# Kernel optimization log

Measured on AMD Instinct MI355X. Metric: run time of the kernel, lower is better.

The kernel has to match this reference:

```python
import jax, jax.numpy as jnp
import numpy as np

B, DZ, H, DY = 4096, 512, 2048, 10
N_STEPS = 64
SCALE = 0.02  # matches param_ulow/uhigh magnitude


def setup_inputs() -> dict:
    key = jax.random.key(0)
    ks = jax.random.split(key, 6)
    x = jax.random.normal(ks[0], (B, DZ), dtype=jnp.float32)
    A = jax.random.normal(ks[1], (DZ, DZ), dtype=jnp.float32) * SCALE
    W1 = jax.random.normal(ks[2], (H, DZ), dtype=jnp.float32) * SCALE
    b1 = jax.random.normal(ks[3], (H,), dtype=jnp.float32) * SCALE
    W2 = jax.random.normal(ks[4], (DY, H), dtype=jnp.float32) * SCALE
    b2 = jax.random.normal(ks[5], (DY,), dtype=jnp.float32) * SCALE
    return {"x": x, "A": A, "W1": W1, "b1": b1, "W2": W2, "b2": b2,
            "n_steps": N_STEPS}


def reference(x, A, W1, b1, W2, b2, n_steps):
    # Z0 = P @ x with P = I  => Z0 = x
    # dz/dt = einsum('ji,bi->bj', A, z) = z @ A.T ; explicit Euler on [0, 1]
    dt = jnp.float32(1.0 / n_steps)

    def euler_step(z, _):
        return z + dt * (z @ A.T), None

    zT, _ = jax.lax.scan(euler_step, x, None, length=n_steps)  # [B, DZ]
    # Q MLP (n_layers=3): Linear -> ReLU -> Linear
    h = jax.nn.relu(zT @ W1.T + b1)  # [B, H]
    y = h @ W2.T + b2                # [B, DY]
    return y
```

## Files before the change

### kernel.cpp

```cpp
#include <hip/hip_runtime.h>
#include <hip/hip_bf16.h>

#define B_SZ 4096
#define DZ   512
#define H_SZ 2048
#define DY   10

#define C2 0.4921875f
#define C3 0.158935546875f
#define C4 0.037872314453125f
#define C5 ((float)(7624512.0/1073741824.0))
#define C6 ((float)(74974368.0/68719476736.0))

typedef __attribute__((ext_vector_type(8))) __bf16 bf16x8;
typedef __attribute__((ext_vector_type(4))) float  f32x4;
typedef __attribute__((ext_vector_type(8))) unsigned short us8;

__device__ inline unsigned short f2bf(float f) {
    unsigned u = __float_as_uint(f);
    u += 0x7fffu + ((u >> 16) & 1u);
    return (unsigned short)(u >> 16);
}
__device__ inline float bf2f(unsigned short s) {
    return __uint_as_float(((unsigned)s) << 16);
}

__device__ __forceinline__ void gl16(const void* g, void* l) {
    __builtin_amdgcn_global_load_lds(
        (const __attribute__((address_space(1))) unsigned int*)(size_t)g,
        (__attribute__((address_space(3))) unsigned int*)(unsigned)(size_t)l,
        16, 0, 0);
}

union SqSmem {
    struct { unsigned short A[64 * 64]; unsigned short B[64 * 64]; } s;
    float epi[64 * 68];
};

__device__ __forceinline__ void stage64(const unsigned short* __restrict__ src,
                                        unsigned short* lds, int row_base,
                                        int kt, int t) {
    const int w = t >> 6, lane = t & 63;
#pragma unroll
    for (int i = 0; i < 2; ++i) {
        int o = w * 128 + i * 64 + lane;
        int row = o >> 3, cc = (o & 7) ^ (row & 7);
        gl16(&src[(size_t)(row_base + row) * 512 + kt * 64 + cc * 8],
             &lds[(size_t)(w * 128 + i * 64) * 8]);
    }
}

#define MFMA_STEP(acc)                                                        \
    {                                                                         \
        _Pragma("unroll")                                                     \
        for (int ks = 0; ks < 2; ++ks) {                                      \
            bf16x8 af[2], bfr[2];                                             \
            _Pragma("unroll")                                                 \
            for (int i = 0; i < 2; ++i) {                                     \
                int ra = wm + i * 16 + l16, ca = (ks * 4 + quad) ^ (ra & 7);  \
                af[i] = *(const bf16x8*)&sm.s.A[ra * 64 + ca * 8];            \
                int rb = wn + i * 16 + l16, cb = (ks * 4 + quad) ^ (rb & 7);  \
                bfr[i] = *(const bf16x8*)&sm.s.B[rb * 64 + cb * 8];           \
            }                                                                 \
            _Pragma("unroll")                                                 \
            for (int i = 0; i < 2; ++i)                                       \
                _Pragma("unroll")                                             \
                for (int j = 0; j < 2; ++j)                                   \
                    acc[i][j] = __builtin_amdgcn_mfma_f32_16x16x32_bf16(      \
                        af[i], bfr[j], acc[i][j], 0, 0, 0);                   \
        }                                                                     \
    }

#define ACC_TO_EPI(acc)                                                       \
    {                                                                         \
        _Pragma("unroll")                                                     \
        for (int i = 0; i < 2; ++i)                                           \
            _Pragma("unroll")                                                 \
            for (int j = 0; j < 2; ++j)                                       \
                _Pragma("unroll")                                             \
                for (int rr = 0; rr < 4; ++rr)                                \
                    sm.epi[(wm + i * 16 + quad * 4 + rr) * 68 +               \
                           wn + j * 16 + l16] = acc[i][j][rr];                \
        __syncthreads();                                                      \
    }

__device__ inline void gemm64_mfma(const unsigned short* __restrict__ Arows,
                                   const unsigned short* __restrict__ Brows,
                                   int m0, int n0, int t, SqSmem& sm) {
    const int lane = t & 63, w = t >> 6, quad = lane >> 4, l16 = lane & 15;
    const int wm = (w & 1) * 32, wn = (w >> 1) * 32;
    f32x4 acc[2][2];
#pragma unroll
    for (int i = 0; i < 2; ++i)
#pragma unroll
        for (int j = 0; j < 2; ++j) acc[i][j] = (f32x4){0.f, 0.f, 0.f, 0.f};
    for (int kt = 0; kt < 8; ++kt) {
        stage64(Arows, sm.s.A, m0, kt, t);
        stage64(Brows, sm.s.B, n0, kt, t);
        __syncthreads();
        MFMA_STEP(acc)
        __syncthreads();
    }
    ACC_TO_EPI(acc)
}

__device__ inline void gemm64_f32src(const float* __restrict__ Arows,
                                     const float* __restrict__ Bsrc,
                                     int m0, int n0, int t, SqSmem& sm) {
    const int lane = t & 63, w = t >> 6, quad = lane >> 4, l16 = lane & 15;
    const int wm = (w & 1) * 32, wn = (w >> 1) * 32;
    const int r = t >> 2, cq = t & 3;
    f32x4 acc[2][2];
#pragma unroll
    for (int i = 0; i < 2; ++i)
#pragma unroll
        for (int j = 0; j < 2; ++j) acc[i][j] = (f32x4){0.f, 0.f, 0.f, 0.f};
    for (int kt = 0; kt < 8; ++kt) {
        float va[16];
#pragma unroll
        for (int u = 0; u < 4; ++u) {
            float4 f = *(const float4*)&Arows[(size_t)(m0 + r) * 512 + kt * 64 + cq * 16 + u * 4];
            va[u * 4 + 0] = f.x; va[u * 4 + 1] = f.y;
            va[u * 4 + 2] = f.z; va[u * 4 + 3] = f.w;
        }
#pragma unroll
        for (int j2 = 0; j2 < 2; ++j2) {
            us8 h;
#pragma unroll
            for (int j = 0; j < 8; ++j) h[j] = f2bf(va[j2 * 8 + j]);
            int cc = cq * 2 + j2;
            *(us8*)&sm.s.A[r * 64 + (cc ^ (r & 7)) * 8] = h;
        }
#pragma unroll
        for (int u = 0; u < 4; ++u) {
            float4 f = *(const float4*)&Bsrc[(size_t)(kt * 64 + r) * 512 + n0 + cq * 16 + u * 4];
            float vv[4] = {f.x, f.y, f.z, f.w};
#pragma unroll
            for (int j = 0; j < 4; ++j) {
                int n = cq * 16 + u * 4 + j;
                sm.s.B[n * 64 + ((r >> 3) ^ (n & 7)) * 8 + (r & 7)] = f2bf(vv[j]);
            }
        }
        __syncthreads();
        MFMA_STEP(acc)
        __syncthreads();
    }
    ACC_TO_EPI(acc)
}

__device__ inline void epi_out_bf(unsigned short* __restrict__ dst, int m0,
                                  int n0, int t, SqSmem& sm) {
    const int r = t >> 2, cq = t & 3;
    us8 h0, h1;
#pragma unroll
    for (int j = 0; j < 8; ++j) {
        h0[j] = f2bf(sm.epi[r * 68 + cq * 16 + j]);
        h1[j] = f2bf(sm.epi[r * 68 + cq * 16 + 8 + j]);
    }
    *(us8*)&dst[(size_t)(m0 + r) * 512 + n0 + cq * 16]     = h0;
    *(us8*)&dst[(size_t)(m0 + r) * 512 + n0 + cq * 16 + 8] = h1;
}
__device__ inline void epi_out_bfT(unsigned short* __restrict__ dst, int m0,
                                   int n0, int t, SqSmem& sm) {
    const int cf = t >> 2, rq = t & 3;
    us8 o0, o1;
#pragma unroll
    for (int i = 0; i < 8; ++i) {
        o0[i] = f2bf(sm.epi[(rq * 16 + i) * 68 + cf]);
        o1[i] = f2bf(sm.epi[(rq * 16 + 8 + i) * 68 + cf]);
    }
    *(us8*)&dst[(size_t)(n0 + cf) * 512 + m0 + rq * 16]     = o0;
    *(us8*)&dst[(size_t)(n0 + cf) * 512 + m0 + rq * 16 + 8] = o1;
}

__global__ __launch_bounds__(256) void k_s1(
    const float* __restrict__ A, const float* __restrict__ x,
    const float* __restrict__ W1, const float* __restrict__ b2,
    unsigned short* __restrict__ A2_bf, unsigned short* __restrict__ A2T_bf,
    unsigned short* __restrict__ AT_bf, unsigned short* __restrict__ x_bf,
    unsigned short* __restrict__ W1_bf, float* __restrict__ y) {
    __shared__ SqSmem sm;
    const int b = blockIdx.x, t = threadIdx.x;

    if (b < 64) {
        const int m0 = (b >> 3) * 64, n0 = (b & 7) * 64;
        gemm64_f32src(A, A, m0, n0, t, sm);
        epi_out_bf(A2_bf, m0, n0, t, sm);
        epi_out_bfT(A2T_bf, m0, n0, t, sm);
    } else if (b < 128) {
        const int bb = b - 64, m0 = (bb >> 3) * 64, n0 = (bb & 7) * 64;
        const int r = t >> 2, cq = t & 3;
#pragma unroll
        for (int u = 0; u < 4; ++u) {
            float4 f = *(const float4*)&A[(size_t)(m0 + r) * 512 + n0 + cq * 16 + u * 4];
            sm.epi[r * 68 + cq * 16 + u * 4 + 0] = f.x;
            sm.epi[r * 68 + cq * 16 + u * 4 + 1] = f.y;
            sm.epi[r * 68 + cq * 16 + u * 4 + 2] = f.z;
            sm.epi[r * 68 + cq * 16 + u * 4 + 3] = f.w;
        }
        __syncthreads();
        epi_out_bfT(AT_bf, m0, n0, t, sm);
    } else {
        const int gid = (b - 128) * 256 + t;
        const float4* x4 = (const float4*)x;
#pragma unroll
        for (int i = 0; i < 8; ++i) {
            int id = gid + i * 32768;
            float4 v0 = x4[(size_t)id * 2], v1 = x4[(size_t)id * 2 + 1];
            us8 o;
            o[0] = f2bf(v0.x); o[1] = f2bf(v0.y); o[2] = f2bf(v0.z); o[3] = f2bf(v0.w);
            o[4] = f2bf(v1.x); o[5] = f2bf(v1.y); o[6] = f2bf(v1.z); o[7] = f2bf(v1.w);
            *(us8*)&x_bf[(size_t)id * 8] = o;
        }
        const float4* w4 = (const float4*)W1;
#pragma unroll
        for (int i = 0; i < 4; ++i) {
            int id = gid + i * 32768;
            float4 v0 = w4[(size_t)id * 2], v1 = w4[(size_t)id * 2 + 1];
            us8 o;
            o[0] = f2bf(v0.x); o[1] = f2bf(v0.y); o[2] = f2bf(v0.z); o[3] = f2bf(v0.w);
            o[4] = f2bf(v1.x); o[5] = f2bf(v1.y); o[6] = f2bf(v1.z); o[7] = f2bf(v1.w);
            *(us8*)&W1_bf[(size_t)id * 8] = o;
        }
#pragma unroll
        for (int i = 0; i < 2; ++i) {
            int id = gid + i * 32768;
            if (id < B_SZ * DY) y[id] = b2[id % 10];
        }
    }
}

__global__ __launch_bounds__(256) void k_s2(
    const unsigned short* __restrict__ W1_bf,
    const unsigned short* __restrict__ A2_bf,
    const unsigned short* __restrict__ A2T_bf,
    const unsigned short* __restrict__ AT_bf,
    unsigned short* __restrict__ A4T_bf, unsigned short* __restrict__ U1_bf,
    unsigned short* __restrict__ U2_bf) {
    __shared__ SqSmem sm;
    const int b = blockIdx.x, t = threadIdx.x;
    if (b < 64) {
        const int m0 = (b >> 3) * 64, n0 = (b & 7) * 64;
        gemm64_mfma(A2T_bf, A2_bf, m0, n0, t, sm);
        epi_out_bf(A4T_bf, m0, n0, t, sm);
    } else if (b < 320) {
        const int bb = b - 64, m0 = (bb >> 3) * 64, n0 = (bb & 7) * 64;
        gemm64_mfma(W1_bf, AT_bf, m0, n0, t, sm);
        epi_out_bf(U1_bf, m0, n0, t, sm);
    } else {
        const int bb = b - 320, m0 = (bb >> 3) * 64, n0 = (bb & 7) * 64;
        gemm64_mfma(W1_bf, A2T_bf, m0, n0, t, sm);
        epi_out_bf(U2_bf, m0, n0, t, sm);
    }
}

__global__ __launch_bounds__(256) void k_s3(
    const float* __restrict__ W1, const unsigned short* __restrict__ U1_bf,
    const unsigned short* __restrict__ U2_bf,
    const unsigned short* __restrict__ A2T_bf,
    const unsigned short* __restrict__ A4T_bf,
    unsigned short* __restrict__ w1f) {
    __shared__ SqSmem sm;
    const int b = blockIdx.x, t = threadIdx.x;
    const int m0 = (b >> 3) * 64, n0 = (b & 7) * 64;
    const int lane = t & 63, w = t >> 6, quad = lane >> 4, l16 = lane & 15;
    const int wm = (w & 1) * 32, wn = (w >> 1) * 32;
    f32x4 acc[2][2];
#pragma unroll
    for (int i = 0; i < 2; ++i)
#pragma unroll
        for (int j = 0; j < 2; ++j) acc[i][j] = (f32x4){0.f, 0.f, 0.f, 0.f};

#pragma unroll
    for (int pass = 0; pass < 2; ++pass) {
        const unsigned short* __restrict__ Bt = pass ? A4T_bf : A2T_bf;
        const float c1c = pass ? C5 : C3;
        const float c2c = pass ? C6 : C4;
        for (int kt = 0; kt < 8; ++kt) {
            stage64(Bt, sm.s.B, n0, kt, t);
#pragma unroll
            for (int c = 0; c < 2; ++c) {
                int idx = c * 256 + t, row = idx >> 3, cc = idx & 7;
                int ccs = cc ^ (row & 7);
                size_t ga = (size_t)(m0 + row) * 512 + kt * 64 + cc * 8;
                us8 u1 = *(const us8*)&U1_bf[ga];
                us8 u2 = *(const us8*)&U2_bf[ga];
                us8 g;
#pragma unroll
                for (int j = 0; j < 8; ++j)
                    g[j] = f2bf(c1c * bf2f(u1[j]) + c2c * bf2f(u2[j]));
                *(us8*)&sm.s.A[row * 64 + ccs * 8] = g;
            }
            __syncthreads();
            MFMA_STEP(acc)
            __syncthreads();
        }
    }
    ACC_TO_EPI(acc)

    const int r = t >> 2, cq = t & 3;
    size_t gbase = (size_t)(m0 + r) * 512 + n0 + cq * 16;
    us8 u1a = *(const us8*)&U1_bf[gbase], u1b = *(const us8*)&U1_bf[gbase + 8];
    us8 u2a = *(const us8*)&U2_bf[gbase], u2b = *(const us8*)&U2_bf[gbase + 8];
    float4 wa = *(const float4*)&W1[gbase],      wbv = *(const float4*)&W1[gbase + 4];
    float4 wc = *(const float4*)&W1[gbase + 8],  wd  = *(const float4*)&W1[gbase + 12];
    float wf[16] = {wa.x, wa.y, wa.z, wa.w, wbv.x, wbv.y, wbv.z, wbv.w,
                    wc.x, wc.y, wc.z, wc.w, wd.x,  wd.y,  wd.z,  wd.w};
    us8 h0, h1;
#pragma unroll
    for (int j = 0; j < 8; ++j) {
        h0[j] = f2bf(wf[j] + bf2f(u1a[j]) + C2 * bf2f(u2a[j]) +
                     sm.epi[r * 68 + cq * 16 + j]);
        h1[j] = f2bf(wf[8 + j] + bf2f(u1b[j]) + C2 * bf2f(u2b[j]) +
                     sm.epi[r * 68 + cq * 16 + 8 + j]);
    }
    *(us8*)&w1f[gbase]     = h0;
    *(us8*)&w1f[gbase + 8] = h1;
}

union SmemU {
    struct { unsigned short A[128 * 64]; unsigned short B[128 * 64]; } s;
    struct { unsigned short h[128 * 136]; } e;
};

__global__ __launch_bounds__(256) void mlp_kernel(
    const unsigned short* __restrict__ x_bf,
    const unsigned short* __restrict__ w1f,
    const float* __restrict__ b1, const float* __restrict__ W2,
    float* __restrict__ y) {
    __shared__ SmemU sm;
    const int t    = threadIdx.x;
    const int lane = t & 63, w = t >> 6;
    const int quad = lane >> 4, l16 = lane & 15;
    const int wm = (w & 1) * 64, wn = (w >> 1) * 64;
    const int m0g = blockIdx.x * 128, n0g = blockIdx.y * 128;

    f32x4 acc[4][4];
#pragma unroll
    for (int i = 0; i < 4; ++i)
#pragma unroll
        for (int j = 0; j < 4; ++j) acc[i][j] = (f32x4){0.f, 0.f, 0.f, 0.f};

    for (int kt = 0; kt < 8; ++kt) {
#pragma unroll
        for (int i = 0; i < 4; ++i) {
            int o = w * 256 + i * 64 + lane;
            int row = o >> 3, cc = (o & 7) ^ (row & 7);
            gl16(&x_bf[(size_t)(m0g + row) * 512 + kt * 64 + cc * 8],
                 &sm.s.A[(size_t)(w * 256 + i * 64) * 8]);
        }
#pragma unroll
        for (int i = 0; i < 4; ++i) {
            int o = w * 256 + i * 64 + lane;
            int row = o >> 3, cc = (o & 7) ^ (row & 7);
            gl16(&w1f[(size_t)(n0g + row) * 512 + kt * 64 + cc * 8],
                 &sm.s.B[(size_t)(w * 256 + i * 64) * 8]);
        }
        __syncthreads();
#pragma unroll
        for (int ks = 0; ks < 2; ++ks) {
            bf16x8 af[4], bfr[4];
#pragma unroll
            for (int i = 0; i < 4; ++i) {
                int ra = wm + i * 16 + l16, ca = (ks * 4 + quad) ^ (ra & 7);
                af[i] = *(const bf16x8*)&sm.s.A[ra * 64 + ca * 8];
                int rb = wn + i * 16 + l16, cb = (ks * 4 + quad) ^ (rb & 7);
                bfr[i] = *(const bf16x8*)&sm.s.B[rb * 64 + cb * 8];
            }
#pragma unroll
            for (int i = 0; i < 4; ++i)
#pragma unroll
                for (int j = 0; j < 4; ++j)
                    acc[i][j] = __builtin_amdgcn_mfma_f32_16x16x32_bf16(
                        af[i], bfr[j], acc[i][j], 0, 0, 0);
        }
        __syncthreads();
    }

    float bias[4];
#pragma unroll
    for (int j = 0; j < 4; ++j) bias[j] = b1[n0g + wn + j * 16 + l16];
#pragma unroll
    for (int i = 0; i < 4; ++i)
#pragma unroll
        for (int j = 0; j < 4; ++j)
#pragma unroll
            for (int r = 0; r < 4; ++r) {
                float h = acc[i][j][r] + bias[j];
                h = h > 0.f ? h : 0.f;
                sm.e.h[(wm + i * 16 + quad * 4 + r) * 136 + wn + j * 16 + l16] =
                    f2bf(h);
            }
    __syncthreads();

    {
        bf16x8 wfrag[4];
#pragma unroll
        for (int kc = 0; kc < 4; ++kc) {
            us8 wb;
            if (l16 < DY) {
                const float* wp = &W2[(size_t)l16 * H_SZ + n0g + kc * 32 + quad * 8];
#pragma unroll
                for (int j = 0; j < 8; ++j) wb[j] = f2bf(wp[j]);
            } else {
#pragma unroll
                for (int j = 0; j < 8; ++j) wb[j] = 0;
            }
            wfrag[kc] = *(bf16x8*)&wb;
        }
#pragma unroll
        for (int hh = 0; hh < 2; ++hh) {
            const int mrow = w * 32 + hh * 16;
            f32x4 ay = (f32x4){0.f, 0.f, 0.f, 0.f};
#pragma unroll
            for (int kc = 0; kc < 4; ++kc) {
                bf16x8 af = *(const bf16x8*)&sm.e.h[(mrow + l16) * 136 +
                                                    kc * 32 + quad * 8];
                ay = __builtin_amdgcn_mfma_f32_16x16x32_bf16(af, wfrag[kc], ay,
                                                             0, 0, 0);
            }
            if (l16 < DY) {
#pragma unroll
                for (int r = 0; r < 4; ++r)
                    atomicAdd(&y[(size_t)(m0g + mrow + quad * 4 + r) * DY + l16],
                              ay[r]);
            }
        }
    }
}

extern "C" void kernel_launch(void* const* d_in, const int* in_sizes, int n_in,
                              void* d_out, int out_size, void* d_ws, size_t ws_size,
                              hipStream_t stream) {
    const float* x  = (const float*)d_in[0];
    const float* A  = (const float*)d_in[1];
    const float* W1 = (const float*)d_in[2];
    const float* b1 = (const float*)d_in[3];
    const float* W2 = (const float*)d_in[4];
    const float* b2 = (const float*)d_in[5];
    float* y = (float*)d_out;

    char* ws = (char*)d_ws;
    const size_t HMB = 512u * 1024, MB = 1u << 20;
    unsigned short* AT_bf  = (unsigned short*)(ws);
    unsigned short* A2_bf  = (unsigned short*)(ws + 1 * HMB);
    unsigned short* A2T_bf = (unsigned short*)(ws + 2 * HMB);
    unsigned short* A4T_bf = (unsigned short*)(ws + 3 * HMB);
    unsigned short* U1_bf  = (unsigned short*)(ws + 2 * MB);
    unsigned short* U2_bf  = (unsigned short*)(ws + 4 * MB);
    unsigned short* w1f    = (unsigned short*)(ws + 6 * MB);
    unsigned short* W1_bf  = (unsigned short*)(ws + 8 * MB);
    unsigned short* x_bf   = (unsigned short*)(ws + 10 * MB);

    k_s1<<<256, 256, 0, stream>>>(A, x, W1, b2, A2_bf, A2T_bf, AT_bf, x_bf,
                                  W1_bf, y);
    k_s2<<<576, 256, 0, stream>>>(W1_bf, A2_bf, A2T_bf, AT_bf, A4T_bf, U1_bf,
                                  U2_bf);
    k_s3<<<256, 256, 0, stream>>>(W1, U1_bf, U2_bf, A2T_bf, A4T_bf, w1f);
    mlp_kernel<<<dim3(32, 16), dim3(256), 0, stream>>>(x_bf, w1f, b1, W2, y);
}
```

Measured before the change: 140.7 us.

## Fold polynomial coefficients into a combined A-power matrix in k_s3

Adds an A^3 (transposed) product in k_s2 and changes k_s3 from two K-passes over U1/U2 to a single pass. The single pass multiplies U2 = W1·A^2 by a combined matrix C3·A + C4·A^2 + C5·A^3 + C6·A^4, built on the fly from the four bf16 A-power tiles. This halves the k_s3 MFMA loop and the per-tile U1/U2 loads. In exchange it adds 64 extra blocks to k_s2 and four small matrix reads per tile, and changes the bf16 rounding path.

After: 133.6 us. 5.1% less time.

```diff
diff --git a/kernel.cpp b/kernel.cpp
--- a/kernel.cpp
+++ b/kernel.cpp
@@ -232,23 +232,28 @@
 
 __global__ __launch_bounds__(256) void k_s2(
     const unsigned short* __restrict__ W1_bf,
+    const unsigned short* __restrict__ A_bfx,
     const unsigned short* __restrict__ A2_bf,
     const unsigned short* __restrict__ A2T_bf,
     const unsigned short* __restrict__ AT_bf,
-    unsigned short* __restrict__ A4T_bf, unsigned short* __restrict__ U1_bf,
-    unsigned short* __restrict__ U2_bf) {
+    unsigned short* __restrict__ A3T_bf, unsigned short* __restrict__ A4T_bf,
+    unsigned short* __restrict__ U1_bf, unsigned short* __restrict__ U2_bf) {
     __shared__ SqSmem sm;
     const int b = blockIdx.x, t = threadIdx.x;
     if (b < 64) {
         const int m0 = (b >> 3) * 64, n0 = (b & 7) * 64;
+        gemm64_mfma(AT_bf, A2_bf, m0, n0, t, sm);
+        epi_out_bf(A3T_bf, m0, n0, t, sm);
+    } else if (b < 128) {
+        const int bb = b - 64, m0 = (bb >> 3) * 64, n0 = (bb & 7) * 64;
         gemm64_mfma(A2T_bf, A2_bf, m0, n0, t, sm);
         epi_out_bf(A4T_bf, m0, n0, t, sm);
-    } else if (b < 320) {
-        const int bb = b - 64, m0 = (bb >> 3) * 64, n0 = (bb & 7) * 64;
+    } else if (b < 384) {
+        const int bb = b - 128, m0 = (bb >> 3) * 64, n0 = (bb & 7) * 64;
         gemm64_mfma(W1_bf, AT_bf, m0, n0, t, sm);
         epi_out_bf(U1_bf, m0, n0, t, sm);
     } else {
-        const int bb = b - 320, m0 = (bb >> 3) * 64, n0 = (bb & 7) * 64;
+        const int bb = b - 384, m0 = (bb >> 3) * 64, n0 = (bb & 7) * 64;
         gemm64_mfma(W1_bf, A2T_bf, m0, n0, t, sm);
         epi_out_bf(U2_bf, m0, n0, t, sm);
     }
@@ -257,7 +262,9 @@
 __global__ __launch_bounds__(256) void k_s3(
     const float* __restrict__ W1, const unsigned short* __restrict__ U1_bf,
     const unsigned short* __restrict__ U2_bf,
+    const unsigned short* __restrict__ AT_bf,
     const unsigned short* __restrict__ A2T_bf,
+    const unsigned short* __restrict__ A3T_bf,
     const unsigned short* __restrict__ A4T_bf,
     unsigned short* __restrict__ w1f) {
     __shared__ SqSmem sm;
@@ -271,30 +278,27 @@
 #pragma unroll
         for (int j = 0; j < 2; ++j) acc[i][j] = (f32x4){0.f, 0.f, 0.f, 0.f};
 
-#pragma unroll
-    for (int pass = 0; pass < 2; ++pass) {
-        const unsigned short* __restrict__ Bt = pass ? A4T_bf : A2T_bf;
-        const float c1c = pass ? C5 : C3;
-        const float c2c = pass ? C6 : C4;
-        for (int kt = 0; kt < 8; ++kt) {
-            stage64(Bt, sm.s.B, n0, kt, t);
-#pragma unroll
-            for (int c = 0; c < 2; ++c) {
-                int idx = c * 256 + t, row = idx >> 3, cc = idx & 7;
-                int ccs = cc ^ (row & 7);
-                size_t ga = (size_t)(m0 + row) * 512 + kt * 64 + cc * 8;
-                us8 u1 = *(const us8*)&U1_bf[ga];
-                us8 u2 = *(const us8*)&U2_bf[ga];
-                us8 g;
-#pragma unroll
-                for (int j = 0; j < 8; ++j)
-                    g[j] = f2bf(c1c * bf2f(u1[j]) + c2c * bf2f(u2[j]));
-                *(us8*)&sm.s.A[row * 64 + ccs * 8] = g;
-            }
-            __syncthreads();
-            MFMA_STEP(acc)
-            __syncthreads();
-        }
+    for (int kt = 0; kt < 8; ++kt) {
+        stage64(U2_bf, sm.s.A, m0, kt, t);
+#pragma unroll
+        for (int c = 0; c < 2; ++c) {
+            int idx = c * 256 + t, row = idx >> 3, cc = idx & 7;
+            int ccs = cc ^ (row & 7);
+            size_t ga = (size_t)(n0 + row) * 512 + kt * 64 + cc * 8;
+            us8 a1 = *(const us8*)&AT_bf[ga];
+            us8 a2 = *(const us8*)&A2T_bf[ga];
+            us8 a3 = *(const us8*)&A3T_bf[ga];
+            us8 a4 = *(const us8*)&A4T_bf[ga];
+            us8 g;
+#pragma unroll
+            for (int j = 0; j < 8; ++j)
+                g[j] = f2bf(C3 * bf2f(a1[j]) + C4 * bf2f(a2[j]) +
+                            C5 * bf2f(a3[j]) + C6 * bf2f(a4[j]));
+            *(us8*)&sm.s.B[row * 64 + ccs * 8] = g;
+        }
+        __syncthreads();
+        MFMA_STEP(acc)
+        __syncthreads();
     }
     ACC_TO_EPI(acc)
 
@@ -445,17 +449,19 @@
     unsigned short* AT_bf  = (unsigned short*)(ws);
     unsigned short* A2_bf  = (unsigned short*)(ws + 1 * HMB);
     unsigned short* A2T_bf = (unsigned short*)(ws + 2 * HMB);
-    unsigned short* A4T_bf = (unsigned short*)(ws + 3 * HMB);
-    unsigned short* U1_bf  = (unsigned short*)(ws + 2 * MB);
-    unsigned short* U2_bf  = (unsigned short*)(ws + 4 * MB);
-    unsigned short* w1f    = (unsigned short*)(ws + 6 * MB);
-    unsigned short* W1_bf  = (unsigned short*)(ws + 8 * MB);
-    unsigned short* x_bf   = (unsigned short*)(ws + 10 * MB);
+    unsigned short* A3T_bf = (unsigned short*)(ws + 3 * HMB);
+    unsigned short* A4T_bf = (unsigned short*)(ws + 4 * HMB);
+    unsigned short* U1_bf  = (unsigned short*)(ws + 3 * MB);
+    unsigned short* U2_bf  = (unsigned short*)(ws + 5 * MB);
+    unsigned short* w1f    = (unsigned short*)(ws + 7 * MB);
+    unsigned short* W1_bf  = (unsigned short*)(ws + 9 * MB);
+    unsigned short* x_bf   = (unsigned short*)(ws + 11 * MB);
 
     k_s1<<<256, 256, 0, stream>>>(A, x, W1, b2, A2_bf, A2T_bf, AT_bf, x_bf,
                                   W1_bf, y);
-    k_s2<<<576, 256, 0, stream>>>(W1_bf, A2_bf, A2T_bf, AT_bf, A4T_bf, U1_bf,
-                                  U2_bf);
-    k_s3<<<256, 256, 0, stream>>>(W1, U1_bf, U2_bf, A2T_bf, A4T_bf, w1f);
+    k_s2<<<640, 256, 0, stream>>>(W1_bf, nullptr, A2_bf, A2T_bf, AT_bf,
+                                  A3T_bf, A4T_bf, U1_bf, U2_bf);
+    k_s3<<<256, 256, 0, stream>>>(W1, U1_bf, U2_bf, AT_bf, A2T_bf, A3T_bf,
+                                  A4T_bf, w1f);
     mlp_kernel<<<dim3(32, 16), dim3(256), 0, stream>>>(x_bf, w1f, b1, W2, y);
 }
```
